# Kernel optimization log

Hardware: AMD Instinct MI355X
Metric: run time of the kernel (lower is better)

Reference implementation:

```python
import jax, jax.numpy as jnp
import numpy as np

B, C, H, W = 2, 48, 128, 256
HEADS = 3
EPS_LN = 1e-6
EPS_NRM = 1e-12


def _conv(x, w, b, padding=0, dilation=1, groups=1):
    # x: NCHW, w: OIHW
    out = jax.lax.conv_general_dilated(
        x, w, window_strides=(1, 1),
        padding=[(padding, padding), (padding, padding)],
        rhs_dilation=(dilation, dilation),
        feature_group_count=groups,
        dimension_numbers=('NCHW', 'OIHW', 'NCHW'))
    return out + b[None, :, None, None]


def _ln2d(x, w, b):
    # LayerNorm over channel dim per pixel (NAFNet-style LayerNorm2d)
    mu = x.mean(axis=1, keepdims=True)
    var = ((x - mu) ** 2).mean(axis=1, keepdims=True)
    return (x - mu) / jnp.sqrt(var + EPS_LN) * w[None, :, None, None] + b[None, :, None, None]


def _l2norm(x):
    # F.normalize(dim=-1): x / max(||x||_2, eps)
    n = jnp.sqrt((x * x).sum(-1, keepdims=True))
    return x / jnp.maximum(n, EPS_NRM)


def setup_inputs() -> dict:
    key = jax.random.key(0)
    ks = iter(jax.random.split(key, 40))
    def nrm(shape, s=0.02):
        return jax.random.normal(next(ks), shape, jnp.float32) * s
    d = {
        'x_l': jax.random.normal(next(ks), (B, C, H, W), jnp.float32),
        'x_r': jax.random.normal(next(ks), (B, C, H, W), jnp.float32),
        'ln1_w': jnp.ones((C,), jnp.float32), 'ln1_b': jnp.zeros((C,), jnp.float32),
        'ln2_w': jnp.ones((C,), jnp.float32), 'ln2_b': jnp.zeros((C,), jnp.float32),
        'qkv_l_w': nrm((3 * C, C, 1, 1)), 'qkv_l_b': jnp.zeros((3 * C,), jnp.float32),
        'qkv_r_w': nrm((3 * C, C, 1, 1)), 'qkv_r_b': jnp.zeros((3 * C,), jnp.float32),
        'dw_l_w': nrm((3 * C, 1, 3, 3)), 'dw_l_b': jnp.zeros((3 * C,), jnp.float32),
        'dw_r_w': nrm((3 * C, 1, 3, 3)), 'dw_r_b': jnp.zeros((3 * C,), jnp.float32),
        'dil0_w': nrm((2 * C, 2 * C, 3, 3)), 'dil0_b': jnp.zeros((2 * C,), jnp.float32),
        'dil1_w': nrm((2 * C, 2 * C, 3, 3)), 'dil1_b': jnp.zeros((2 * C,), jnp.float32),
        'dil2_w': nrm((2 * C, 2 * C, 3, 3)), 'dil2_b': jnp.zeros((2 * C,), jnp.float32),
        'convQ_w': nrm((C, 6 * C, 1, 1)), 'convQ_b': jnp.zeros((C,), jnp.float32),
        'conv1_w': nrm((C, C, 1, 1)), 'conv1_b': jnp.zeros((C,), jnp.float32),
        'conv2_w': nrm((C, C, 1, 1)), 'conv2_b': jnp.zeros((C,), jnp.float32),
        'temperature': jnp.ones((HEADS, 1, 1), jnp.float32),
    }
    return d


def reference(x_l, x_r, ln1_w, ln1_b, ln2_w, ln2_b,
              qkv_l_w, qkv_l_b, qkv_r_w, qkv_r_b,
              dw_l_w, dw_l_b, dw_r_w, dw_r_b,
              dil0_w, dil0_b, dil1_w, dil1_b, dil2_w, dil2_b,
              convQ_w, convQ_b, conv1_w, conv1_b, conv2_w, conv2_b,
              temperature):
    b, c, h, w = x_l.shape
    hw = h * w
    ch = c // HEADS  # channels per head

    norm_l = _ln2d(x_l, ln1_w, ln1_b)
    norm_r = _ln2d(x_r, ln2_w, ln2_b)

    qkvl = _conv(_conv(norm_l, qkv_l_w, qkv_l_b), dw_l_w, dw_l_b, padding=1, groups=3 * c)
    qkvr = _conv(_conv(norm_r, qkv_r_w, qkv_r_b), dw_r_w, dw_r_b, padding=1, groups=3 * c)
    Q_l, K_l, V_l = jnp.split(qkvl, 3, axis=1)
    Q_r, K_r, V_r = jnp.split(qkvr, 3, axis=1)

    Q = jnp.concatenate((Q_l, Q_r), axis=1)  # [b, 2c, h, w]
    Q = jnp.concatenate((
        _conv(Q, dil0_w, dil0_b, padding=2, dilation=2),
        _conv(Q, dil1_w, dil1_b, padding=4, dilation=4),
        _conv(Q, dil2_w, dil2_b, padding=6, dilation=6)), axis=1)  # [b, 6c, h, w]
    Q = _conv(Q, convQ_w, convQ_b)  # [b, c, h, w]

    def heads(t):
        return t.reshape(b, HEADS, ch, hw)

    Q = _l2norm(heads(Q))
    K_l = _l2norm(heads(K_l))
    K_r = _l2norm(heads(K_r))
    V_l = heads(V_l)
    V_r = heads(V_r)

    # channel attention: [b, head, ch, ch]
    A_r2l = jax.nn.softmax(jnp.einsum('bhcn,bhdn->bhcd', Q, K_r) * temperature, axis=-1)
    A_l2r = jax.nn.softmax(jnp.einsum('bhcn,bhdn->bhcd', Q, K_l) * temperature, axis=-1)

    F_l = jnp.einsum('bhcd,bhdn->bhcn', A_r2l, V_l).reshape(b, c, h, w)
    F_r = jnp.einsum('bhcd,bhdn->bhcn', A_l2r, V_r).reshape(b, c, h, w)

    F_l = _conv(F_l, conv1_w, conv1_b)
    F_r = _conv(F_r, conv2_w, conv2_b)
    return (x_l + F_l, x_r + F_r)
```

## Files before the change

### kernel.cpp

```cpp
#include <hip/hip_runtime.h>
#include <hip/hip_bf16.h>

typedef __hip_bfloat16 bf16;
typedef __attribute__((ext_vector_type(8))) short short8;
typedef __attribute__((ext_vector_type(4))) float f32x4;

constexpr int IMG_H = 128;
constexpr int IMG_W = 256;
constexpr int HW    = IMG_H * IMG_W;
constexpr int BB    = 2;
constexpr int CC    = 48;
constexpr int C3    = 144;
constexpr int XPW   = 268;
constexpr int XOFF  = 6;

constexpr int WO_QKVL_W = 0;
constexpr int WO_QKVR_W = 6912;
constexpr int WO_DWL_W  = 13824;
constexpr int WO_DWR_W  = 15120;
constexpr int WO_C1_W   = 16416;
constexpr int WO_C2_W   = 18720;
constexpr int WO_QKVL_B = 21024;
constexpr int WO_QKVR_B = 21168;
constexpr int WO_DWL_B  = 21312;
constexpr int WO_DWR_B  = 21456;
constexpr int WO_C1_B   = 21600;
constexpr int WO_C2_B   = 21648;
constexpr int WO_LN1W   = 21696;
constexpr int WO_LN1B   = 21744;
constexpr int WO_LN2W   = 21792;
constexpr int WO_LN2B   = 21840;
constexpr int WO_TEMP   = 21888;
constexpr int WO_WQ     = 21952;
constexpr int WO_D0W    = 35776;
constexpr int WO_D1W    = 118720;
constexpr int WO_D2W    = 201664;
constexpr int WO_BQ     = 284608;
constexpr int WO_B0     = 284656;
constexpr int WO_B1     = 284752;
constexpr int WO_B2     = 284848;
constexpr int WO_WPACK  = 284944;
constexpr int WO_EFFB   = 409360;
constexpr int WO_NQ     = 409424;
constexpr int WO_NKL    = 409520;
constexpr int WO_NKR    = 409616;
constexpr int WO_AR2L   = 409712;
constexpr int WO_AL2R   = 411248;
constexpr int WO_M1     = 412800;
constexpr int WO_M2     = 417408;
constexpr int WO_WQP    = 422016;
constexpr int WO_PART   = 431232;

constexpr size_t ACT_BASE_BYTES = 2118144;

constexpr size_t A_P  = 0;
constexpr size_t A_Q1 = 9437184;
constexpr size_t A_Q2 = 18874368;
constexpr size_t A_QC = 28311552;

struct PrepArgs {
  const void* src[25];
  int dst[25];
  int n[25];
};

__device__ __forceinline__ bool probe_bf16(const void* ln1w) {
  return ((const unsigned short*)ln1w)[0] == 0x3F80;
}

__global__ __launch_bounds__(256) void prep_k(PrepArgs a, float* __restrict__ wsf) {
  bool isb = probe_bf16(a.src[12]);
  int t = blockIdx.y;
  int i = blockIdx.x * 256 + threadIdx.x;
  if (i < a.n[t]) {
    float v = isb ? __bfloat162float(((const bf16*)a.src[t])[i])
                  : ((const float*)a.src[t])[i];
    wsf[a.dst[t] + i] = v;
  }
}

__global__ __launch_bounds__(512) void effw2_k(const float* __restrict__ wsf,
                                               bf16* __restrict__ wpack) {
  int d  = blockIdx.x / 96;
  int ci = blockIdx.x % 96;
  __shared__ float wds[864];
  __shared__ float wqs[48 * 97];
  const int wdb = (d == 0) ? WO_D0W : (d == 1) ? WO_D1W : WO_D2W;
  for (int idx = threadIdx.x; idx < 864; idx += 512) {
    int m = idx / 9, tt = idx % 9;
    wds[idx] = wsf[wdb + (m * 96 + ci) * 9 + tt];
  }
  for (int idx = threadIdx.x; idx < 4608; idx += 512) {
    int co = idx / 96, m = idx % 96;
    wqs[co * 97 + m] = wsf[WO_WQ + co * 288 + d * 96 + m];
  }
  __syncthreads();
  int tco = threadIdx.x;
  if (tco < 432) {
    int t = tco / 48, co = tco % 48;
    float s = 0.f;
#pragma unroll 8
    for (int m = 0; m < 96; ++m) s += wqs[co * 97 + m] * wds[m * 9 + t];
    int trow = t / 3, dxi = t % 3;
    int ti = (trow == 0) ? (2 - d) * 3 + dxi
           : (trow == 1) ? 9 + d * 3 + dxi
                         : 18 + d * 3 + dxi;
    int kc = ci >> 5, j = ci & 7;
    int L = ((ci & 31) >> 3) * 16 + (co & 15);
    int nt = co >> 4;
    int f = (ti * 3 + kc) * 3 + nt;
    wpack[(size_t)f * 512 + L * 8 + j] = __float2bfloat16(s);
  }
}

__global__ __launch_bounds__(64) void effb_k(const float* __restrict__ wsf,
                                             float* __restrict__ effb) {
  int co = threadIdx.x;
  if (co >= 48) return;
  float s = wsf[WO_BQ + co];
  for (int m = 0; m < 96; ++m) {
    s += wsf[WO_WQ + co * 288 + m]       * wsf[WO_B0 + m];
    s += wsf[WO_WQ + co * 288 + 96 + m]  * wsf[WO_B1 + m];
    s += wsf[WO_WQ + co * 288 + 192 + m] * wsf[WO_B2 + m];
  }
  effb[co] = s;
}

__global__ __launch_bounds__(256) void wqp_k(const float* __restrict__ wsf,
                                             bf16* __restrict__ wqp) {
  int idx = blockIdx.x * 256 + threadIdx.x;
  if (idx >= 18432) return;
  int side = idx / 9216;
  int rem = idx % 9216;
  int nt = rem / 1024;
  int kt = (rem / 512) % 2;
  int e  = rem % 512;
  int L = e >> 3, j = e & 7;
  int o = nt * 16 + (L & 15);
  int kp = kt * 32 + (L >> 4) * 8 + j;
  int g = kp >> 4, r = kp & 15;
  float val = 0.f;
  if (r < 12) {
    int c = g * 12 + r;
    val = wsf[(side ? WO_QKVR_W : WO_QKVL_W) + o * 48 + c];
  }
  wqp[idx] = __float2bfloat16(val);
}

__global__ __launch_bounds__(256) void lnqkv_k(
    const void* __restrict__ x, const void* __restrict__ probe,
    const float* __restrict__ lnw, const float* __restrict__ lnb,
    const bf16* __restrict__ wqp_side, const float* __restrict__ qb,
    bf16* __restrict__ pre) {
  __shared__ __align__(16) unsigned char LDSU[21504 + 18432];
  bf16* XNs = (bf16*)LDSU;
  float2* red = (float2*)(LDSU + 9216);
  bf16* Cs = (bf16*)LDSU;
  bf16* W = (bf16*)(LDSU + 21504);
  int tid = threadIdx.x;
  for (int i = tid; i < 1152; i += 256)
    ((uint4*)W)[i] = ((const uint4*)wqp_side)[i];

  int px = tid & 63;
  int w = tid >> 6;
  int p = blockIdx.x * 64 + px;
  int b = p >> 15;
  int pix = p & (HW - 1);
  size_t base = (size_t)b * CC * HW + pix;
  float v[12];
  if (probe_bf16(probe)) {
    const bf16* xp = (const bf16*)x + base;
#pragma unroll
    for (int c = 0; c < 12; ++c)
      v[c] = __bfloat162float(xp[(size_t)(w * 12 + c) * HW]);
  } else {
    const float* xp = (const float*)x + base;
#pragma unroll
    for (int c = 0; c < 12; ++c) v[c] = xp[(size_t)(w * 12 + c) * HW];
  }
  float s = 0.f, s2 = 0.f;
#pragma unroll
  for (int c = 0; c < 12; ++c) { s += v[c]; s2 += v[c] * v[c]; }
  red[w * 64 + px] = make_float2(s, s2);
  __syncthreads();
  float S = 0.f, S2 = 0.f;
#pragma unroll
  for (int i = 0; i < 4; ++i) {
    float2 r2 = red[i * 64 + px];
    S += r2.x; S2 += r2.y;
  }
  float mu = S * (1.f / 48.f);
  float var = S2 * (1.f / 48.f) - mu * mu;
  float rs = rsqrtf(var + 1e-6f);
  bf16 o16[16];
#pragma unroll
  for (int c = 0; c < 12; ++c)
    o16[c] = __float2bfloat16((v[c] - mu) * rs * lnw[w * 12 + c] + lnb[w * 12 + c]);
#pragma unroll
  for (int c = 12; c < 16; ++c) o16[c] = __float2bfloat16(0.f);
  *(uint4*)(XNs + px * 72 + w * 16) = *(uint4*)(o16);
  *(uint4*)(XNs + px * 72 + w * 16 + 8) = *(uint4*)(o16 + 8);
  __syncthreads();

  int L = tid & 63;
  int lo = L & 15, hi = L >> 4;
  const bf16* arow = XNs + (size_t)(w * 16 + lo) * 72 + hi * 8;
  short8 a0 = *(const short8*)(arow);
  short8 a1 = *(const short8*)(arow + 32);
  __syncthreads();
#pragma unroll
  for (int nt = 0; nt < 9; ++nt) {
    float bvv = qb[nt * 16 + lo];
    f32x4 acc = {bvv, bvv, bvv, bvv};
    acc = __builtin_amdgcn_mfma_f32_16x16x32_bf16(
        a0, *(const short8*)(W + (nt * 2 + 0) * 512 + L * 8), acc, 0, 0, 0);
    acc = __builtin_amdgcn_mfma_f32_16x16x32_bf16(
        a1, *(const short8*)(W + (nt * 2 + 1) * 512 + L * 8), acc, 0, 0, 0);
#pragma unroll
    for (int r = 0; r < 4; ++r)
      Cs[(nt * 16 + lo) * 66 + w * 16 + hi * 4 + r] = __float2bfloat16(acc[r]);
  }
  __syncthreads();
  int pix0 = (blockIdx.x * 64) & (HW - 1);
#pragma unroll
  for (int pass = 0; pass < 18; ++pass) {
    int o = pass * 8 + (tid >> 5);
    int px2 = (tid & 31) * 2;
    bf16 t2[2];
    t2[0] = Cs[o * 66 + px2];
    t2[1] = Cs[o * 66 + px2 + 1];
    *(unsigned*)(pre + ((size_t)(b * C3 + o)) * HW + pix0 + px2) = *(unsigned*)t2;
  }
}

__global__ __launch_bounds__(256) void dw_k(
    const bf16* __restrict__ in, const float* __restrict__ w9,
    const float* __restrict__ bias, bf16* __restrict__ out) {
  int gid = blockIdx.x;
  int yt = gid & 15;
  int c = (gid >> 4) % C3;
  int b = gid / (16 * C3);
  int ry = threadIdx.x >> 5, xi = threadIdx.x & 31;
  int y = yt * 8 + ry;
  int x0 = xi * 8;
  const bf16* base = in + ((size_t)(b * C3 + c)) * HW;
  float wv[9];
#pragma unroll
  for (int t = 0; t < 9; ++t) wv[t] = w9[c * 9 + t];
  float bz = bias[c];
  float acc[8];
#pragma unroll
  for (int i = 0; i < 8; ++i) acc[i] = bz;
#pragma unroll
  for (int ky = 0; ky < 3; ++ky) {
    int yy = y + ky - 1;
    if ((unsigned)yy >= (unsigned)IMG_H) continue;
    const bf16* row = base + yy * IMG_W + x0;
    uint4 m = *(const uint4*)(row);
    float f[10];
    f[0] = (x0 > 0) ? __bfloat162float(row[-1]) : 0.f;
    f[9] = (x0 + 8 < IMG_W) ? __bfloat162float(row[8]) : 0.f;
    f[1] = __uint_as_float(m.x << 16);
    f[2] = __uint_as_float(m.x & 0xFFFF0000u);
    f[3] = __uint_as_float(m.y << 16);
    f[4] = __uint_as_float(m.y & 0xFFFF0000u);
    f[5] = __uint_as_float(m.z << 16);
    f[6] = __uint_as_float(m.z & 0xFFFF0000u);
    f[7] = __uint_as_float(m.w << 16);
    f[8] = __uint_as_float(m.w & 0xFFFF0000u);
    float w0 = wv[ky * 3], w1 = wv[ky * 3 + 1], w2 = wv[ky * 3 + 2];
#pragma unroll
    for (int i = 0; i < 8; ++i)
      acc[i] += w0 * f[i] + w1 * f[i + 1] + w2 * f[i + 2];
  }
  bf16 o[8];
#pragma unroll
  for (int i = 0; i < 8; ++i) o[i] = __float2bfloat16(acc[i]);
  *(uint4*)(out + ((size_t)(b * C3 + c)) * HW + y * IMG_W + x0) = *(uint4*)o;
}

__global__ __launch_bounds__(256) void qc_k(const bf16* __restrict__ q1,
                                            const bf16* __restrict__ q2,
                                            bf16* __restrict__ qc) {
  int b = blockIdx.x >> 7;
  int y = blockIdx.x & 127;
  int half = blockIdx.y;
  int tid = threadIdx.x;
  int x0 = half * 128;
  int px = tid & 127;
  int cig = tid >> 7;
  __shared__ __align__(16) bf16 T[128][100];
#pragma unroll 8
  for (int k = 0; k < 48; ++k) {
    int ci = cig * 48 + k;
    const bf16* src = (ci < 48)
        ? q1 + (((size_t)(b * C3 + ci)) * IMG_H + y) * IMG_W
        : q2 + (((size_t)(b * C3 + ci - 48)) * IMG_H + y) * IMG_W;
    T[px][ci] = src[x0 + px];
  }
  __syncthreads();
  size_t rowbase = ((size_t)(b * IMG_H + y)) * XPW * 96 + (size_t)half * 12864;
#pragma unroll 1
  for (int i = 0; i < 13; ++i) {
    int e4 = i * 256 + tid;
    if (e4 >= 3216) break;
    int e = e4 * 4;
    int xp = (e + half * 12864) / 96;
    int ci = (e + half * 12864) % 96;
    int x = xp - XOFF;
    uint2 val;
    if ((unsigned)x < (unsigned)IMG_W) {
      val = *(const uint2*)(&T[x - x0][ci]);
    } else {
      val.x = 0u; val.y = 0u;
    }
    *(uint2*)(qc + rowbase + e) = val;
  }
}

__global__ __launch_bounds__(256, 1) void dil_mfma_k(
    const bf16* __restrict__ qc, const bf16* __restrict__ wp,
    const float* __restrict__ effb, bf16* __restrict__ qh) {
  __shared__ __align__(16) unsigned char LDSU[74176];
  bf16* Arow = (bf16*)LDSU;
  bf16* Wb   = (bf16*)(LDSU + 55744);
  float* Cs  = (float*)LDSU;

  int bid = blockIdx.x;
  int xcd = bid & 7;
  int slot = bid >> 3;
  int y = xcd * 16 + (slot & 15);
  int b = slot >> 4;
  int tid = threadIdx.x;
  int L = tid & 63;
  int w = tid >> 6;
  int lo = L & 15, hi = L >> 4;

  f32x4 acc[4][3];
#pragma unroll
  for (int g2 = 0; g2 < 4; ++g2)
#pragma unroll
    for (int nt = 0; nt < 3; ++nt) {
      float bv = effb[nt * 16 + lo];
      acc[g2][nt] = {bv, bv, bv, bv};
    }

  {
    const uint4* ws = (const uint4*)wp;
    uint4* wd = (uint4*)Wb;
    wd[tid] = ws[tid];
    wd[tid + 256] = ws[tid + 256];
    if (tid < 64) wd[tid + 512] = ws[tid + 512];
  }

  int dy_prev = -100;
#pragma unroll 1
  for (int g = 0; g < 9; ++g) {
    int D = (g < 3) ? (6 - 2 * g) : (g < 6) ? (2 * (g - 2)) : (2 * (g - 5));
    int dy = (g < 3) ? -D : (g < 6) ? 0 : D;
    int yy = y + dy;
    bool valid = (unsigned)yy < (unsigned)IMG_H;
    if (valid && dy != dy_prev) {
      const uint4* src = (const uint4*)(qc + (size_t)(b * IMG_H + yy) * (XPW * 96));
      uint4 abuf[13];
#pragma unroll
      for (int r = 0; r < 13; ++r) {
        int i = tid + r * 256;
        if (i < 3216) abuf[r] = src[i];
      }
      __syncthreads();
#pragma unroll
      for (int r = 0; r < 13; ++r) {
        int i = tid + r * 256;
        if (i < 3216) {
          int px = i / 12;
          int cr = i - px * 12;
          *(uint4*)(Arow + px * 104 + cr * 8) = abuf[r];
        }
      }
    }
    dy_prev = dy;
#pragma unroll 1
    for (int dxi = 0; dxi < 3; ++dxi) {
      int ti = g * 3 + dxi;
      uint4 w0, w1, w2;
      if (ti < 26) {
        const uint4* ws = (const uint4*)(wp + (ti + 1) * 4608);
        w0 = ws[tid];
        w1 = ws[tid + 256];
        if (tid < 64) w2 = ws[tid + 512];
      }
      __syncthreads();
      if (valid) {
        const bf16* wb = Wb + (ti & 1) * 4608;
        short8 bfr[9];
#pragma unroll
        for (int f = 0; f < 9; ++f)
          bfr[f] = *(const short8*)(wb + f * 512 + L * 8);
        int dx = (dxi - 1) * D;
        const bf16* ar = Arow + (XOFF + dx + w * 64 + lo) * 104 + hi * 8;
#pragma unroll
        for (int g2 = 0; g2 < 4; ++g2)
#pragma unroll
          for (int kc = 0; kc < 3; ++kc) {
            short8 a = *(const short8*)(ar + g2 * (16 * 104) + kc * 32);
#pragma unroll
            for (int nt = 0; nt < 3; ++nt)
              acc[g2][nt] = __builtin_amdgcn_mfma_f32_16x16x32_bf16(
                  a, bfr[kc * 3 + nt], acc[g2][nt], 0, 0, 0);
          }
      }
      if (ti < 26) {
        uint4* wd = (uint4*)(Wb + ((ti + 1) & 1) * 4608);
        wd[tid] = w0;
        wd[tid + 256] = w1;
        if (tid < 64) wd[tid + 512] = w2;
      }
    }
  }

  __syncthreads();
#pragma unroll
  for (int g2 = 0; g2 < 4; ++g2)
#pragma unroll
    for (int nt = 0; nt < 3; ++nt)
#pragma unroll
      for (int r = 0; r < 4; ++r)
        Cs[(nt * 16 + lo) * 260 + w * 64 + g2 * 16 + hi * 4 + r] = acc[g2][nt][r];
  __syncthreads();
  size_t obase = (size_t)b * CC * HW + (size_t)y * IMG_W;
#pragma unroll 1
  for (int i = 0; i < 12; ++i) {
    int chunk = i * 256 + tid;
    int co = chunk >> 6;
    int px4 = (chunk & 63) * 4;
    const float* s = Cs + co * 260 + px4;
    bf16 t4[4];
    t4[0] = __float2bfloat16(s[0]);
    t4[1] = __float2bfloat16(s[1]);
    t4[2] = __float2bfloat16(s[2]);
    t4[3] = __float2bfloat16(s[3]);
    *(uint2*)(qh + obase + (size_t)co * HW + px4) = *(uint2*)t4;
  }
}

__device__ __forceinline__ float wave_sum(float v) {
#pragma unroll
  for (int off = 32; off > 0; off >>= 1) v += __shfl_down(v, off, 64);
  return v;
}

__device__ __forceinline__ float blo(unsigned u) {
  return __uint_as_float(u << 16);
}
__device__ __forceinline__ float bhi(unsigned u) {
  return __uint_as_float(u & 0xFFFF0000u);
}

__global__ __launch_bounds__(256) void rownorm_k(
    const bf16* __restrict__ qh, const bf16* __restrict__ qkvl,
    const bf16* __restrict__ qkvr, float* __restrict__ nq,
    float* __restrict__ nkl, float* __restrict__ nkr) {
  int id = blockIdx.x;
  int which = id / 96;
  int rid = id % 96;
  int b = rid / 48;
  int c = rid % 48;
  const bf16* ptr = (which == 0) ? qh + ((size_t)(b * CC + c)) * HW
                  : (which == 1) ? qkvl + ((size_t)(b * C3 + 48 + c)) * HW
                                 : qkvr + ((size_t)(b * C3 + 48 + c)) * HW;
  float s = 0.f;
#pragma unroll 2
  for (int it = 0; it < 16; ++it) {
    int n0 = (it * 256 + threadIdx.x) * 8;
    uint4 u = *(const uint4*)(ptr + n0);
    float a0 = blo(u.x), a1 = bhi(u.x), a2 = blo(u.y), a3 = bhi(u.y);
    float a4 = blo(u.z), a5 = bhi(u.z), a6 = blo(u.w), a7 = bhi(u.w);
    s += a0 * a0 + a1 * a1 + a2 * a2 + a3 * a3 + a4 * a4 + a5 * a5 +
         a6 * a6 + a7 * a7;
  }
  s = wave_sum(s);
  __shared__ float red[4];
  if ((threadIdx.x & 63) == 0) red[threadIdx.x >> 6] = s;
  __syncthreads();
  if (threadIdx.x == 0) {
    float tot = red[0] + red[1] + red[2] + red[3];
    float* dst = (which == 0) ? nq : (which == 1) ? nkl : nkr;
    dst[rid] = tot;
  }
}

__global__ __launch_bounds__(256) void logits_mfma_k(
    const bf16* __restrict__ qh, const bf16* __restrict__ qkvl,
    const bf16* __restrict__ qkvr, float* __restrict__ part) {
  int abh = blockIdx.x;
  int chunk = blockIdx.y;
  int a = abh / 6;
  int b = (abh / 3) % 2;
  int h = abh % 3;
  int tid = threadIdx.x;
  int L = tid & 63, w = tid >> 6;
  int lo = L & 15, hi = L >> 4;
  const bf16* qrow = qh + ((size_t)(b * CC + h * 16 + lo)) * HW;
  const bf16* krow =
      ((a == 0) ? qkvr : qkvl) + ((size_t)(b * C3 + 48 + h * 16 + lo)) * HW;
  int px0 = chunk * 1024 + w * 256 + hi * 8;
  f32x4 acc = {0.f, 0.f, 0.f, 0.f};
#pragma unroll
  for (int s = 0; s < 8; ++s) {
    short8 av = *(const short8*)(qrow + px0 + s * 32);
    short8 bv = *(const short8*)(krow + px0 + s * 32);
    acc = __builtin_amdgcn_mfma_f32_16x16x32_bf16(av, bv, acc, 0, 0, 0);
  }
  __shared__ float red[4][256];
#pragma unroll
  for (int r = 0; r < 4; ++r) red[w][(hi * 4 + r) * 16 + lo] = acc[r];
  __syncthreads();
  float sum = red[0][tid] + red[1][tid] + red[2][tid] + red[3][tid];
  part[((size_t)abh * 32 + chunk) * 256 + tid] = sum;
}

__global__ __launch_bounds__(256) void logits_red_k(
    const float* __restrict__ part, const float* __restrict__ nq,
    const float* __restrict__ nkl, const float* __restrict__ nkr,
    const float* __restrict__ temp, float* __restrict__ logr2l,
    float* __restrict__ logl2r) {
  int abh = blockIdx.x;
  int a = abh / 6, b = (abh / 3) % 2, h = abh % 3;
  int t = threadIdx.x;
  int i = t >> 4, j = t & 15;
  float s = 0.f;
  const float* p = part + (size_t)abh * 32 * 256 + t;
#pragma unroll 8
  for (int c = 0; c < 32; ++c) s += p[c * 256];
  float qn = fmaxf(sqrtf(nq[b * 48 + h * 16 + i]), 1e-12f);
  float kn = fmaxf(sqrtf(((a == 0) ? nkr : nkl)[b * 48 + h * 16 + j]), 1e-12f);
  float val = s / (qn * kn) * temp[h];
  ((a == 0) ? logr2l : logl2r)[b * 768 + h * 256 + i * 16 + j] = val;
}

__global__ __launch_bounds__(256) void softmaxM_k(float* __restrict__ wsf) {
  int tid = threadIdx.x;
  __shared__ float A1[1536], A2[1536];
  if (tid < 192) {
    const float* p = wsf + ((tid < 96) ? WO_AR2L : WO_AL2R) + (tid % 96) * 16;
    float* dst = ((tid < 96) ? A1 : A2) + (tid % 96) * 16;
    float m = -1e30f;
#pragma unroll
    for (int j = 0; j < 16; ++j) m = fmaxf(m, p[j]);
    float s = 0.f;
    float e[16];
#pragma unroll
    for (int j = 0; j < 16; ++j) {
      e[j] = expf(p[j] - m);
      s += e[j];
    }
    float inv = 1.f / s;
#pragma unroll
    for (int j = 0; j < 16; ++j) dst[j] = e[j] * inv;
  }
  __syncthreads();
#pragma unroll 1
  for (int idx = tid; idx < 4608; idx += 256) {
    int b = idx / 2304;
    int r = idx % 2304;
    int o = r / 48;
    int cp = r % 48;
    int h = cp >> 4, j = cp & 15;
    const float* a1 = &A1[((b * 3 + h) * 16) * 16 + j];
    const float* a2 = &A2[((b * 3 + h) * 16) * 16 + j];
    float s1 = 0.f, s2 = 0.f;
#pragma unroll
    for (int i = 0; i < 16; ++i) {
      s1 += wsf[WO_C1_W + o * 48 + h * 16 + i] * a1[i * 16];
      s2 += wsf[WO_C2_W + o * 48 + h * 16 + i] * a2[i * 16];
    }
    wsf[WO_M1 + idx] = s1;
    wsf[WO_M2 + idx] = s2;
  }
}

__global__ __launch_bounds__(256) void attn_out2_k(
    const bf16* __restrict__ q1, const bf16* __restrict__ q2,
    const void* __restrict__ x1, const void* __restrict__ x2,
    const void* __restrict__ probe, const float* __restrict__ Mall,
    const float* __restrict__ cball, void* __restrict__ out) {
  int side = blockIdx.z;
  const bf16* qkv = side ? q2 : q1;
  const void* x = side ? x2 : x1;
  const float* M = Mall + side * 4608;
  const float* cb = cball + side * 48;
  int tid = threadIdx.x;
  int p = blockIdx.x * 256 + tid;
  int b = __builtin_amdgcn_readfirstlane(p >> 15);
  int pix = p & (HW - 1);
  int o0 = blockIdx.y * 16;
  bool isb = probe_bf16(probe);

  float v[CC];
  const bf16* vb = qkv + ((size_t)(b * C3 + 96)) * HW + pix;
#pragma unroll
  for (int c = 0; c < CC; ++c) v[c] = __bfloat162float(vb[(size_t)c * HW]);

  const float* Mb = M + b * 2304;
  size_t base = (size_t)b * CC * HW + pix;
  float res[16];
#pragma unroll 2
  for (int o = 0; o < 16; ++o) {
    float acc = cb[o0 + o];
    const float* mrow = Mb + (o0 + o) * 48;
#pragma unroll
    for (int c = 0; c < CC; ++c) acc += mrow[c] * v[c];
    res[o] = acc;
  }
  size_t obase = (size_t)side * BB * CC * HW + base + (size_t)o0 * HW;
  if (isb) {
    const bf16* xp = (const bf16*)x + base + (size_t)o0 * HW;
    bf16* op = (bf16*)out + obase;
#pragma unroll
    for (int o = 0; o < 16; ++o)
      op[(size_t)o * HW] =
          __float2bfloat16(res[o] + __bfloat162float(xp[(size_t)o * HW]));
  } else {
    const float* xp = (const float*)x + base + (size_t)o0 * HW;
    float* op = (float*)out + obase;
#pragma unroll
    for (int o = 0; o < 16; ++o) op[(size_t)o * HW] = res[o] + xp[(size_t)o * HW];
  }
}

extern "C" void kernel_launch(void* const* d_in, const int* in_sizes, int n_in,
                              void* d_out, int out_size, void* d_ws, size_t ws_size,
                              hipStream_t stream) {
  (void)in_sizes; (void)n_in; (void)out_size; (void)ws_size;
  const void* x_l = d_in[0];
  const void* x_r = d_in[1];
  const void* probe = d_in[2];
  float* wsf = (float*)d_ws;
  bf16* wpack = (bf16*)(wsf + WO_WPACK);
  bf16* wqp = (bf16*)(wsf + WO_WQP);
  bf16* act = (bf16*)((char*)d_ws + ACT_BASE_BYTES);
  bf16* P  = act + A_P;
  bf16* Q1 = act + A_Q1;
  bf16* Q2 = act + A_Q2;
  bf16* QC = act + A_QC;
  bf16* qh = P;

  PrepArgs pa;
  const int srcIdx[25] = {6, 8, 10, 12, 22, 24, 7, 9, 11, 13, 23, 25,
                          2, 3, 4, 5, 26, 20, 14, 16, 18, 21, 15, 17, 19};
  const int dstOff[25] = {WO_QKVL_W, WO_QKVR_W, WO_DWL_W, WO_DWR_W, WO_C1_W, WO_C2_W,
                          WO_QKVL_B, WO_QKVR_B, WO_DWL_B, WO_DWR_B, WO_C1_B, WO_C2_B,
                          WO_LN1W, WO_LN1B, WO_LN2W, WO_LN2B, WO_TEMP,
                          WO_WQ, WO_D0W, WO_D1W, WO_D2W, WO_BQ, WO_B0, WO_B1, WO_B2};
  const int ns[25] = {6912, 6912, 1296, 1296, 2304, 2304, 144, 144, 144, 144,
                      48, 48, 48, 48, 48, 48, 3,
                      13824, 82944, 82944, 82944, 48, 96, 96, 96};
  for (int i = 0; i < 25; ++i) {
    pa.src[i] = d_in[srcIdx[i]];
    pa.dst[i] = dstOff[i];
    pa.n[i] = ns[i];
  }
  prep_k<<<dim3(324, 25), 256, 0, stream>>>(pa, wsf);

  effw2_k<<<288, 512, 0, stream>>>(wsf, wpack);
  effb_k<<<1, 64, 0, stream>>>(wsf, wsf + WO_EFFB);
  wqp_k<<<72, 256, 0, stream>>>(wsf, wqp);

  lnqkv_k<<<1024, 256, 0, stream>>>(x_l, probe, wsf + WO_LN1W, wsf + WO_LN1B,
                                    wqp, wsf + WO_QKVL_B, P);
  dw_k<<<BB * C3 * 16, 256, 0, stream>>>(P, wsf + WO_DWL_W, wsf + WO_DWL_B, Q1);
  lnqkv_k<<<1024, 256, 0, stream>>>(x_r, probe, wsf + WO_LN2W, wsf + WO_LN2B,
                                    wqp + 9216, wsf + WO_QKVR_B, P);
  dw_k<<<BB * C3 * 16, 256, 0, stream>>>(P, wsf + WO_DWR_W, wsf + WO_DWR_B, Q2);

  qc_k<<<dim3(BB * IMG_H, 2), 256, 0, stream>>>(Q1, Q2, QC);

  dil_mfma_k<<<256, 256, 0, stream>>>(QC, wpack, wsf + WO_EFFB, qh);

  rownorm_k<<<288, 256, 0, stream>>>(qh, Q1, Q2, wsf + WO_NQ,
                                     wsf + WO_NKL, wsf + WO_NKR);
  logits_mfma_k<<<dim3(12, 32), 256, 0, stream>>>(qh, Q1, Q2, wsf + WO_PART);
  logits_red_k<<<12, 256, 0, stream>>>(wsf + WO_PART, wsf + WO_NQ,
                                       wsf + WO_NKL, wsf + WO_NKR,
                                       wsf + WO_TEMP, wsf + WO_AR2L,
                                       wsf + WO_AL2R);
  softmaxM_k<<<1, 256, 0, stream>>>(wsf);

  attn_out2_k<<<dim3(256, 3, 2), 256, 0, stream>>>(
      Q1, Q2, x_l, x_r, probe, wsf + WO_M1, wsf + WO_C1_B, d_out);
}
```

Measured before the change: 300.3 us.

## Load dilated-conv weights to registers and stage input rows via direct global-to-LDS

Weight fragments for the dilated-conv MFMA kernel are now loaded by each lane straight from global memory into registers and software-prefetched one tap ahead, which removes the LDS weight double buffer and the per-tap barrier. Input rows are copied to LDS with global_load_lds (direct global-to-LDS DMA) instead of a staging pass through registers, and the padded 104-element pitch becomes an unpadded 96 to match the contiguous copy. This cuts register pressure from the abuf staging and reduces LDS footprint and synchronisation. The unpadded pitch may bring back LDS bank conflicts on the A-fragment reads, and each wave now reads the weights redundantly from global or L2.

```diff
diff --git a/kernel.cpp b/kernel.cpp
--- a/kernel.cpp
+++ b/kernel.cpp
@@ -4,6 +4,7 @@
 typedef __hip_bfloat16 bf16;
 typedef __attribute__((ext_vector_type(8))) short short8;
 typedef __attribute__((ext_vector_type(4))) float f32x4;
+typedef unsigned int u32;
 
 constexpr int IMG_H = 128;
 constexpr int IMG_W = 256;
@@ -321,9 +322,8 @@
 __global__ __launch_bounds__(256, 1) void dil_mfma_k(
     const bf16* __restrict__ qc, const bf16* __restrict__ wp,
     const float* __restrict__ effb, bf16* __restrict__ qh) {
-  __shared__ __align__(16) unsigned char LDSU[74176];
+  __shared__ __align__(16) unsigned char LDSU[51456];
   bf16* Arow = (bf16*)LDSU;
-  bf16* Wb   = (bf16*)(LDSU + 55744);
   float* Cs  = (float*)LDSU;
 
   int bid = blockIdx.x;
@@ -345,13 +345,11 @@
       acc[g2][nt] = {bv, bv, bv, bv};
     }
 
-  {
-    const uint4* ws = (const uint4*)wp;
-    uint4* wd = (uint4*)Wb;
-    wd[tid] = ws[tid];
-    wd[tid + 256] = ws[tid + 256];
-    if (tid < 64) wd[tid + 512] = ws[tid + 512];
-  }
+  const bf16* wrow = wp + L * 8;
+  short8 wc[9];
+#pragma unroll
+  for (int f = 0; f < 9; ++f)
+    wc[f] = *(const short8*)(wrow + f * 512);
 
   int dy_prev = -100;
 #pragma unroll 1
@@ -361,60 +359,51 @@
     int yy = y + dy;
     bool valid = (unsigned)yy < (unsigned)IMG_H;
     if (valid && dy != dy_prev) {
-      const uint4* src = (const uint4*)(qc + (size_t)(b * IMG_H + yy) * (XPW * 96));
-      uint4 abuf[13];
+      __syncthreads();
+      const bf16* src = qc + (size_t)(b * IMG_H + yy) * (XPW * 96);
 #pragma unroll
       for (int r = 0; r < 13; ++r) {
-        int i = tid + r * 256;
-        if (i < 3216) abuf[r] = src[i];
+        int c = w + r * 4;
+        if (c < 51) {
+          int i = c * 64 + L;
+          if (i < 3216) {
+            __builtin_amdgcn_global_load_lds(
+                (const __attribute__((address_space(1))) u32*)(src + (size_t)i * 8),
+                (__attribute__((address_space(3))) u32*)(Arow + (size_t)c * 512),
+                16, 0, 0);
+          }
+        }
       }
       __syncthreads();
-#pragma unroll
-      for (int r = 0; r < 13; ++r) {
-        int i = tid + r * 256;
-        if (i < 3216) {
-          int px = i / 12;
-          int cr = i - px * 12;
-          *(uint4*)(Arow + px * 104 + cr * 8) = abuf[r];
-        }
-      }
+      dy_prev = dy;
     }
-    dy_prev = dy;
-#pragma unroll 1
+#pragma unroll
     for (int dxi = 0; dxi < 3; ++dxi) {
       int ti = g * 3 + dxi;
-      uint4 w0, w1, w2;
+      short8 wn[9];
       if (ti < 26) {
-        const uint4* ws = (const uint4*)(wp + (ti + 1) * 4608);
-        w0 = ws[tid];
-        w1 = ws[tid + 256];
-        if (tid < 64) w2 = ws[tid + 512];
+        const bf16* wr = wrow + (ti + 1) * 4608;
+#pragma unroll
+        for (int f = 0; f < 9; ++f)
+          wn[f] = *(const short8*)(wr + f * 512);
       }
-      __syncthreads();
       if (valid) {
-        const bf16* wb = Wb + (ti & 1) * 4608;
-        short8 bfr[9];
-#pragma unroll
-        for (int f = 0; f < 9; ++f)
-          bfr[f] = *(const short8*)(wb + f * 512 + L * 8);
         int dx = (dxi - 1) * D;
-        const bf16* ar = Arow + (XOFF + dx + w * 64 + lo) * 104 + hi * 8;
+        const bf16* ar = Arow + (size_t)(XOFF + dx + w * 64 + lo) * 96 + hi * 8;
 #pragma unroll
         for (int g2 = 0; g2 < 4; ++g2)
 #pragma unroll
           for (int kc = 0; kc < 3; ++kc) {
-            short8 a = *(const short8*)(ar + g2 * (16 * 104) + kc * 32);
+            short8 a = *(const short8*)(ar + g2 * (16 * 96) + kc * 32);
 #pragma unroll
             for (int nt = 0; nt < 3; ++nt)
               acc[g2][nt] = __builtin_amdgcn_mfma_f32_16x16x32_bf16(
-                  a, bfr[kc * 3 + nt], acc[g2][nt], 0, 0, 0);
+                  a, wc[kc * 3 + nt], acc[g2][nt], 0, 0, 0);
           }
       }
       if (ti < 26) {
-        uint4* wd = (uint4*)(Wb + ((ti + 1) & 1) * 4608);
-        wd[tid] = w0;
-        wd[tid + 256] = w1;
-        if (tid < 64) wd[tid + 512] = w2;
+#pragma unroll
+        for (int f = 0; f < 9; ++f) wc[f] = wn[f];
       }
     }
   }
```

After: 275.0 us. 8.4% less time.
